# Optimization experiments

Measured on AMD Instinct MI355X. Metric: run time of the kernel, lower is better.

The kernel has to match this reference:

```python
import jax, jax.numpy as jnp
import numpy as np

NHEAD = 6
EPS = 1.1920929e-07  # torch RMSNorm default eps = finfo(float32).eps


def _rms(x, g):
    return x * jax.lax.rsqrt(jnp.mean(x * x, axis=-1, keepdims=True) + EPS) * g


def _mha(q, k, v):
    # q: [B, Sq, Hq, D]; k, v: [B, Sk, Hk, D] with Hk == Hq or Hk == 1 (broadcast)
    d = q.shape[-1]
    qh = q.transpose(0, 2, 1, 3)            # [B, Hq, Sq, D]
    kh = k.transpose(0, 2, 1, 3)            # [B, Hk, Sk, D]
    vh = v.transpose(0, 2, 1, 3)
    s = jnp.matmul(qh, kh.transpose(0, 1, 3, 2)) * (1.0 / np.sqrt(d).astype(np.float32))
    a = jax.nn.softmax(s, axis=-1)
    return jnp.matmul(a, vh).transpose(0, 2, 1, 3)  # [B, Sq, Hq, D]


def setup_inputs() -> dict:
    key = jax.random.key(0)
    B, R, G, E, L = 4, 1024, 8, 192, 4
    F = 2 * E  # dim_feedforward = emsize * 2
    ks = jax.random.split(key, 12)

    def w(k, shape):
        return jax.random.normal(k, shape, jnp.float32) * 0.02

    return {
        "hidden": jax.random.normal(ks[0], (B, R, G, E), jnp.float32),
        "Wq1": w(ks[1], (L, E, E)), "Wk1": w(ks[2], (L, E, E)),
        "Wv1": w(ks[3], (L, E, E)), "Wo1": w(ks[4], (L, E, E)),
        "Wq2": w(ks[5], (L, E, E)), "Wk2": w(ks[6], (L, E, E)),
        "Wv2": w(ks[7], (L, E, E)), "Wo2": w(ks[8], (L, E, E)),
        "W1": w(ks[9], (L, E, F)), "W2": w(ks[10], (L, F, E)),
        "g1": jnp.ones((L, E), jnp.float32),
        "g2": jnp.ones((L, E), jnp.float32),
        "g3": jnp.ones((L, E), jnp.float32),
        "single_eval_pos": 768,
    }


def reference(hidden, Wq1, Wk1, Wv1, Wo1, Wq2, Wk2, Wv2, Wo2, W1, W2, g1, g2, g3, single_eval_pos):
    B, R, G, E = hidden.shape
    H, D = NHEAD, E // NHEAD
    sep = int(single_eval_pos)
    L = Wq1.shape[0]
    x = hidden
    for i in range(L):
        # --- per-sample attention between feature groups: seqs of length G ---
        xf = x.reshape(B * R, G, E)
        q = (xf @ Wq1[i]).reshape(B * R, G, H, D)
        k = (xf @ Wk1[i]).reshape(B * R, G, H, D)
        v = (xf @ Wv1[i]).reshape(B * R, G, H, D)
        xf = xf + _mha(q, k, v).reshape(B * R, G, E) @ Wo1[i]
        # --- along-column attention over rows with train/test split ---
        xr = _rms(xf, g1[i]).reshape(B, R, G, E).transpose(0, 2, 1, 3).reshape(B * G, R, E)
        q = (xr @ Wq2[i]).reshape(B * G, R, H, D)
        k = (xr[:, :sep] @ Wk2[i]).reshape(B * G, sep, H, D)
        v = (xr[:, :sep] @ Wv2[i]).reshape(B * G, sep, H, D)
        train_out = _mha(q[:, :sep], k, v)
        # test rows attend to first head's keys/values only (broadcast over heads)
        test_out = _mha(q[:, sep:], k[:, :, :1], v[:, :, :1])
        attn = jnp.concatenate([train_out, test_out], axis=1).reshape(B * G, R, E) @ Wo2[i]
        xc = _rms(xr + attn, g2[i])
        # --- MLP (exact GELU) + final RMSNorm ---
        x = xc.reshape(B, G, R, E).transpose(0, 2, 1, 3)
        x = x + jax.nn.gelu(x @ W1[i], approximate=False) @ W2[i]
        x = _rms(x, g3[i])
    return x
```

## Files before the change

kernel.cpp:

```cpp
#include <hip/hip_runtime.h>
#include <hip/hip_bf16.h>
#include <math.h>

#define B_ 4
#define R_ 1024
#define G_ 8
#define E_ 192
#define H_ 6
#define D_ 32
#define L_ 4
#define F_ 384
#define M_ (B_*R_*G_)
static const size_t NBUF = (size_t)M_ * E_;
static const size_t WPL  = 8 * (size_t)E_ * E_ + 2 * (size_t)E_ * F_;

typedef __attribute__((ext_vector_type(8))) short bf16x8;
typedef __attribute__((ext_vector_type(8))) unsigned short u16x8;
typedef __attribute__((ext_vector_type(4))) float f32x4;

__device__ __forceinline__ float gelu_exact(float x) {
    return 0.5f * x * (1.0f + erff(x * 0.7071067811865475f));
}
__device__ __forceinline__ unsigned short f2bf(float f) {
    __hip_bfloat16 h = __float2bfloat16(f);
    return *(unsigned short*)&h;
}
__device__ __forceinline__ float bf2f(unsigned short h) {
    union { unsigned u; float f; } v; v.u = ((unsigned)h) << 16; return v.f;
}
__device__ __forceinline__ bf16x8 mk8(unsigned long long lo, unsigned long long hi) {
    union { unsigned long long q[2]; bf16x8 v; } u;
    u.q[0] = lo; u.q[1] = hi; return u.v;
}

__global__ __launch_bounds__(256)
void k_convw_all(const float* __restrict__ Wq1, const float* __restrict__ Wk1,
                 const float* __restrict__ Wv1, const float* __restrict__ Wo1,
                 const float* __restrict__ Wq2, const float* __restrict__ Wk2,
                 const float* __restrict__ Wv2, const float* __restrict__ Wo2,
                 const float* __restrict__ W1,  const float* __restrict__ W2,
                 unsigned short* __restrict__ Wt)
{
    const int t = blockIdx.x;
    const int layer = t / 432;
    const int r = t % 432;
    const float* src; unsigned short* dst; int K, N; float scale = 1.f; int tile;
    if (r < 288) {
        const int w = r / 36; tile = r % 36; K = E_; N = E_;
        const float* tab[8] = {Wq1, Wk1, Wv1, Wo1, Wq2, Wk2, Wv2, Wo2};
        src = tab[w] + (size_t)layer * E_ * E_;
        dst = Wt + (size_t)layer * WPL + (size_t)w * E_ * E_;
        if (w == 0) scale = 0.17677669529663687f;
        if (w == 4) scale = 0.17677669529663687f * 1.4426950408889634f;
    } else if (r < 360) {
        tile = r - 288; K = E_; N = F_;
        src = W1 + (size_t)layer * E_ * F_;
        dst = Wt + (size_t)layer * WPL + 8 * (size_t)E_ * E_;
    } else {
        tile = r - 360; K = F_; N = E_;
        src = W2 + (size_t)layer * E_ * F_;
        dst = Wt + (size_t)layer * WPL + 8 * (size_t)E_ * E_ + (size_t)E_ * F_;
    }
    const int ntx = N / 32;
    const int kb = (tile / ntx) * 32, nb = (tile % ntx) * 32;
    __shared__ float tl[32][33];
    const int tx = threadIdx.x & 31, ty = threadIdx.x >> 5;
    for (int i2 = 0; i2 < 32; i2 += 8)
        tl[ty + i2][tx] = src[(size_t)(kb + ty + i2) * N + nb + tx];
    __syncthreads();
    for (int i2 = 0; i2 < 32; i2 += 8)
        dst[(size_t)(nb + ty + i2) * K + kb + tx] = f2bf(tl[tx][ty + i2] * scale);
}

template<bool ABF16, int EPI>
__global__ __launch_bounds__(256)
void k_gemm_mfma(const void* __restrict__ Ap, const unsigned short* __restrict__ Wt,
                 void* __restrict__ Cp, int ldc, int K)
{
    __shared__ unsigned short As[64][40];
    __shared__ unsigned short Bs[192][40];
    const int m0 = blockIdx.x * 64;
    const int n0 = blockIdx.y * 192;
    const int tid = threadIdx.x;
    const int w = tid >> 6, lane = tid & 63, l15 = lane & 15, g = lane >> 4;
    const int arow = tid >> 2, akoff = (tid & 3) << 3;
    f32x4 acc[4][3];
#pragma unroll
    for (int mt = 0; mt < 4; ++mt)
#pragma unroll
        for (int nt = 0; nt < 3; ++nt)
#pragma unroll
            for (int r2 = 0; r2 < 4; ++r2) acc[mt][nt][r2] = 0.f;
    const int nK = K >> 5;

    float4 ax, ay; u16x8 av; u16x8 bv0, bv1, bv2;
    auto gload = [&](int k0) {
        if (ABF16) {
            av = *(const u16x8*)((const unsigned short*)Ap + (size_t)(m0 + arow) * K + k0 + akoff);
        } else {
            const float* ap = (const float*)Ap + (size_t)(m0 + arow) * K + k0 + akoff;
            ax = *(const float4*)ap; ay = *(const float4*)(ap + 4);
        }
        bv0 = *(const u16x8*)(Wt + (size_t)(n0 + arow      ) * K + k0 + akoff);
        bv1 = *(const u16x8*)(Wt + (size_t)(n0 + arow +  64) * K + k0 + akoff);
        bv2 = *(const u16x8*)(Wt + (size_t)(n0 + arow + 128) * K + k0 + akoff);
    };
    auto swrite = [&]() {
        u16x8 aw;
        if (ABF16) aw = av;
        else {
            aw[0] = f2bf(ax.x); aw[1] = f2bf(ax.y); aw[2] = f2bf(ax.z); aw[3] = f2bf(ax.w);
            aw[4] = f2bf(ay.x); aw[5] = f2bf(ay.y); aw[6] = f2bf(ay.z); aw[7] = f2bf(ay.w);
        }
        *(u16x8*)&As[arow][akoff] = aw;
        *(u16x8*)&Bs[arow][akoff] = bv0;
        *(u16x8*)&Bs[arow + 64][akoff] = bv1;
        *(u16x8*)&Bs[arow + 128][akoff] = bv2;
    };

    gload(0);
    for (int kc = 0; kc < nK; ++kc) {
        __syncthreads();
        swrite();
        __syncthreads();
        if (kc + 1 < nK) gload((kc + 1) << 5);
        bf16x8 af[4], bfr[3];
#pragma unroll
        for (int mt = 0; mt < 4; ++mt) af[mt] = *(const bf16x8*)&As[mt * 16 + l15][g * 8];
#pragma unroll
        for (int nt = 0; nt < 3; ++nt) bfr[nt] = *(const bf16x8*)&Bs[w * 48 + nt * 16 + l15][g * 8];
#pragma unroll
        for (int mt = 0; mt < 4; ++mt)
#pragma unroll
            for (int nt = 0; nt < 3; ++nt)
                acc[mt][nt] = __builtin_amdgcn_mfma_f32_16x16x32_bf16(af[mt], bfr[nt], acc[mt][nt], 0, 0, 0);
    }

#pragma unroll
    for (int mt = 0; mt < 4; ++mt)
#pragma unroll
        for (int r2 = 0; r2 < 4; ++r2) {
            const int m = m0 + mt * 16 + g * 4 + r2;
#pragma unroll
            for (int nt = 0; nt < 3; ++nt) {
                const int n = w * 48 + nt * 16 + l15;
                float v = acc[mt][nt][r2];
                if (EPI == 1) v = gelu_exact(v);
                ((unsigned short*)Cp)[(size_t)m * ldc + n0 + n] = f2bf(v);
            }
        }
}

template<bool RESBF16, int EPI>
__global__ __launch_bounds__(256)
void k_gemm_rms32(const unsigned short* __restrict__ Ap, const unsigned short* __restrict__ Wt,
                  const void* __restrict__ Resp, const float* __restrict__ gvec,
                  void* __restrict__ Cp, int K)
{
    __shared__ unsigned short As[32][40];
    __shared__ unsigned short Bs[192][40];
    __shared__ float ss_red[4][16];
    const int m0 = blockIdx.x * 32;
    const int tid = threadIdx.x;
    const int w = tid >> 6, lane = tid & 63, l15 = lane & 15, g = lane >> 4;
    const int mt = w & 1, nh = w >> 1;
    const int arow = tid >> 2, akoff = (tid & 3) << 3;
    f32x4 acc[6];
#pragma unroll
    for (int nt = 0; nt < 6; ++nt)
#pragma unroll
        for (int r2 = 0; r2 < 4; ++r2) acc[nt][r2] = 0.f;
    const int nK = K >> 5;

    u16x8 av, bv0, bv1, bv2;
    auto gload = [&](int k0) {
        if (tid < 128)
            av = *(const u16x8*)(Ap + (size_t)(m0 + arow) * K + k0 + akoff);
        bv0 = *(const u16x8*)(Wt + (size_t)(arow      ) * K + k0 + akoff);
        bv1 = *(const u16x8*)(Wt + (size_t)(arow +  64) * K + k0 + akoff);
        bv2 = *(const u16x8*)(Wt + (size_t)(arow + 128) * K + k0 + akoff);
    };
    auto swrite = [&]() {
        if (tid < 128) *(u16x8*)&As[arow][akoff] = av;
        *(u16x8*)&Bs[arow][akoff] = bv0;
        *(u16x8*)&Bs[arow + 64][akoff] = bv1;
        *(u16x8*)&Bs[arow + 128][akoff] = bv2;
    };

    gload(0);
    for (int kc = 0; kc < nK; ++kc) {
        __syncthreads();
        swrite();
        __syncthreads();
        if (kc + 1 < nK) gload((kc + 1) << 5);
        bf16x8 af = *(const bf16x8*)&As[mt * 16 + l15][g * 8];
        bf16x8 bfr[6];
#pragma unroll
        for (int nt = 0; nt < 6; ++nt) bfr[nt] = *(const bf16x8*)&Bs[nh * 96 + nt * 16 + l15][g * 8];
#pragma unroll
        for (int nt = 0; nt < 6; ++nt)
            acc[nt] = __builtin_amdgcn_mfma_f32_16x16x32_bf16(af, bfr[nt], acc[nt], 0, 0, 0);
    }

    float ssp[4] = {0.f, 0.f, 0.f, 0.f};
#pragma unroll
    for (int r2 = 0; r2 < 4; ++r2) {
        const int m = m0 + mt * 16 + g * 4 + r2;
#pragma unroll
        for (int nt = 0; nt < 6; ++nt) {
            const int n = nh * 96 + nt * 16 + l15;
            float rres = RESBF16 ? bf2f(((const unsigned short*)Resp)[(size_t)m * E_ + n])
                                 : ((const float*)Resp)[(size_t)m * E_ + n];
            float v = acc[nt][r2] + rres;
            acc[nt][r2] = v;
            ssp[r2] += v * v;
        }
    }
#pragma unroll
    for (int off = 1; off < 16; off <<= 1)
#pragma unroll
        for (int r2 = 0; r2 < 4; ++r2)
            ssp[r2] += __shfl_xor(ssp[r2], off);
    if (l15 == 0) {
#pragma unroll
        for (int r2 = 0; r2 < 4; ++r2)
            ss_red[w][g * 4 + r2] = ssp[r2];
    }
    __syncthreads();
#pragma unroll
    for (int r2 = 0; r2 < 4; ++r2) {
        const int lr = g * 4 + r2;
        const float ss = ss_red[mt][lr] + ss_red[2 + mt][lr];
        const float inv = rsqrtf(ss * (1.0f / 192.0f) + 1.1920929e-07f);
        const int m = m0 + mt * 16 + lr;
        size_t orow;
        if (EPI == 2) {
            const int b = m >> 13, rr = (m >> 3) & 1023, gg = m & 7;
            orow = (((size_t)b * G_ + gg) << 10) + rr;
        } else if (EPI == 3) {
            const int b = m >> 13, gg = (m >> 10) & 7, rr = m & 1023;
            orow = ((((size_t)b << 10) + rr) << 3) + gg;
        } else {
            orow = m;
        }
#pragma unroll
        for (int nt = 0; nt < 6; ++nt) {
            const int n = nh * 96 + nt * 16 + l15;
            const float v = acc[nt][r2] * inv * gvec[n];
            if (EPI == 4) ((float*)Cp)[orow * E_ + n] = v;
            else          ((unsigned short*)Cp)[orow * E_ + n] = f2bf(v);
        }
    }
}

template<bool AF32>
__global__ __launch_bounds__(256)
void k_featblock(const void* __restrict__ Xin, const unsigned short* __restrict__ Wqkv,
                 const unsigned short* __restrict__ Wo, const float* __restrict__ gvec,
                 unsigned short* __restrict__ Ynb)
{
    __shared__ __align__(16) unsigned char raw[576 * 40 * 2];
    __shared__ __align__(16) unsigned short As[32][40];
    __shared__ __align__(16) unsigned short Tl[32][200];
    __shared__ float ss_red[4][32];

    unsigned short (*Bq)[40]    = (unsigned short (*)[40])raw;
    unsigned short (*QKVl)[584] = (unsigned short (*)[584])raw;
    unsigned short (*Bo)[40]    = (unsigned short (*)[40])raw;

    const int m0 = blockIdx.x * 32;
    const int tid = threadIdx.x;
    const int w = tid >> 6, lane = tid & 63, l15 = lane & 15, g = lane >> 4;
    const int arow = (tid & 127) >> 2, akoff = (tid & 3) << 3;

    f32x4 acc[2][9];
#pragma unroll
    for (int mt = 0; mt < 2; ++mt)
#pragma unroll
        for (int nt = 0; nt < 9; ++nt)
#pragma unroll
            for (int r2 = 0; r2 < 4; ++r2) acc[mt][nt][r2] = 0.f;

    u16x8 av; u16x8 bv[9];
    auto gload1 = [&](int k0) {
        if (tid < 128) {
            if (AF32) {
                const float* ap = (const float*)Xin + (size_t)(m0 + arow) * E_ + k0 + akoff;
                float4 x = *(const float4*)ap, y = *(const float4*)(ap + 4);
                av[0] = f2bf(x.x); av[1] = f2bf(x.y); av[2] = f2bf(x.z); av[3] = f2bf(x.w);
                av[4] = f2bf(y.x); av[5] = f2bf(y.y); av[6] = f2bf(y.z); av[7] = f2bf(y.w);
            } else {
                av = *(const u16x8*)((const unsigned short*)Xin + (size_t)(m0 + arow) * E_ + k0 + akoff);
            }
        }
#pragma unroll
        for (int j = 0; j < 9; ++j) {
            const int v = tid + 256 * j;
            bv[j] = *(const u16x8*)(Wqkv + (size_t)(v >> 2) * E_ + k0 + ((v & 3) << 3));
        }
    };
    auto swrite1 = [&]() {
        if (tid < 128) *(u16x8*)&As[arow][akoff] = av;
#pragma unroll
        for (int j = 0; j < 9; ++j) {
            const int v = tid + 256 * j;
            *(u16x8*)&Bq[v >> 2][(v & 3) << 3] = bv[j];
        }
    };

    gload1(0);
    for (int kc = 0; kc < 6; ++kc) {
        __syncthreads();
        swrite1();
        __syncthreads();
        if (kc + 1 < 6) gload1((kc + 1) << 5);
        bf16x8 af0 = *(const bf16x8*)&As[l15][g * 8];
        bf16x8 af1 = *(const bf16x8*)&As[16 + l15][g * 8];
#pragma unroll
        for (int nt = 0; nt < 9; ++nt) {
            bf16x8 bf = *(const bf16x8*)&Bq[w * 144 + nt * 16 + l15][g * 8];
            acc[0][nt] = __builtin_amdgcn_mfma_f32_16x16x32_bf16(af0, bf, acc[0][nt], 0, 0, 0);
            acc[1][nt] = __builtin_amdgcn_mfma_f32_16x16x32_bf16(af1, bf, acc[1][nt], 0, 0, 0);
        }
    }
    __syncthreads();
#pragma unroll
    for (int mt = 0; mt < 2; ++mt)
#pragma unroll
        for (int r2 = 0; r2 < 4; ++r2)
#pragma unroll
            for (int nt = 0; nt < 9; ++nt)
                QKVl[mt * 16 + g * 4 + r2][w * 144 + nt * 16 + l15] = f2bf(acc[mt][nt][r2]);

    u16x8 bo[3];
    auto gload3 = [&](int k0) {
#pragma unroll
        for (int j = 0; j < 3; ++j) {
            const int v = tid + 256 * j;
            bo[j] = *(const u16x8*)(Wo + (size_t)(v >> 2) * E_ + k0 + ((v & 3) << 3));
        }
    };
    gload3(0);
    __syncthreads();

    {
        const int i = lane >> 3, j = lane & 7;
        const int r0 = w * 8;
#pragma unroll
        for (int h = 0; h < 6; ++h) {
            float s = 0.f;
#pragma unroll
            for (int d8 = 0; d8 < 4; ++d8) {
                u16x8 qv = *(const u16x8*)&QKVl[r0 + i][h * 32 + d8 * 8];
                u16x8 kv = *(const u16x8*)&QKVl[r0 + j][192 + h * 32 + d8 * 8];
#pragma unroll
                for (int e = 0; e < 8; ++e) s += bf2f(qv[e]) * bf2f(kv[e]);
            }
            float mx = s;
#pragma unroll
            for (int off = 1; off < 8; off <<= 1) mx = fmaxf(mx, __shfl_xor(mx, off));
            float p = __expf(s - mx);
            float sum = p;
#pragma unroll
            for (int off = 1; off < 8; off <<= 1) sum += __shfl_xor(sum, off);
            p /= sum;
            const int base = lane & ~7;
            float o0 = 0.f, o1 = 0.f, o2 = 0.f, o3 = 0.f;
#pragma unroll
            for (int jj = 0; jj < 8; ++jj) {
                float pj = __shfl(p, base + jj);
                ushort4 vv = *(const ushort4*)&QKVl[r0 + jj][384 + h * 32 + j * 4];
                o0 += pj * bf2f(vv.x); o1 += pj * bf2f(vv.y);
                o2 += pj * bf2f(vv.z); o3 += pj * bf2f(vv.w);
            }
            ushort4 ov; ov.x = f2bf(o0); ov.y = f2bf(o1); ov.z = f2bf(o2); ov.w = f2bf(o3);
            *(ushort4*)&Tl[r0 + i][h * 32 + j * 4] = ov;
        }
    }

    float rv[2][4][3];
#pragma unroll
    for (int mt = 0; mt < 2; ++mt)
#pragma unroll
        for (int r2 = 0; r2 < 4; ++r2) {
            const int m = m0 + mt * 16 + g * 4 + r2;
#pragma unroll
            for (int nt = 0; nt < 3; ++nt) {
                const int n = w * 48 + nt * 16 + l15;
                rv[mt][r2][nt] = AF32 ? ((const float*)Xin)[(size_t)m * E_ + n]
                                      : bf2f(((const unsigned short*)Xin)[(size_t)m * E_ + n]);
            }
        }
    __syncthreads();

    f32x4 acc2[2][3];
#pragma unroll
    for (int mt = 0; mt < 2; ++mt)
#pragma unroll
        for (int nt = 0; nt < 3; ++nt)
#pragma unroll
            for (int r2 = 0; r2 < 4; ++r2) acc2[mt][nt][r2] = 0.f;

    for (int kc = 0; kc < 6; ++kc) {
        __syncthreads();
#pragma unroll
        for (int j = 0; j < 3; ++j) {
            const int v = tid + 256 * j;
            *(u16x8*)&Bo[v >> 2][(v & 3) << 3] = bo[j];
        }
        __syncthreads();
        if (kc + 1 < 6) gload3((kc + 1) << 5);
        const int k0 = kc << 5;
        bf16x8 af0 = *(const bf16x8*)&Tl[l15][k0 + g * 8];
        bf16x8 af1 = *(const bf16x8*)&Tl[16 + l15][k0 + g * 8];
#pragma unroll
        for (int nt = 0; nt < 3; ++nt) {
            bf16x8 bf = *(const bf16x8*)&Bo[w * 48 + nt * 16 + l15][g * 8];
            acc2[0][nt] = __builtin_amdgcn_mfma_f32_16x16x32_bf16(af0, bf, acc2[0][nt], 0, 0, 0);
            acc2[1][nt] = __builtin_amdgcn_mfma_f32_16x16x32_bf16(af1, bf, acc2[1][nt], 0, 0, 0);
        }
    }
    __syncthreads();

    float ssp[2][4] = {};
#pragma unroll
    for (int mt = 0; mt < 2; ++mt)
#pragma unroll
        for (int r2 = 0; r2 < 4; ++r2) {
#pragma unroll
            for (int nt = 0; nt < 3; ++nt) {
                float v = acc2[mt][nt][r2] + rv[mt][r2][nt];
                acc2[mt][nt][r2] = v;
                ssp[mt][r2] += v * v;
            }
        }
#pragma unroll
    for (int off = 1; off < 16; off <<= 1)
#pragma unroll
        for (int mt = 0; mt < 2; ++mt)
#pragma unroll
            for (int r2 = 0; r2 < 4; ++r2)
                ssp[mt][r2] += __shfl_xor(ssp[mt][r2], off);
    if (l15 == 0) {
#pragma unroll
        for (int mt = 0; mt < 2; ++mt)
#pragma unroll
            for (int r2 = 0; r2 < 4; ++r2)
                ss_red[w][mt * 16 + g * 4 + r2] = ssp[mt][r2];
    }
    __syncthreads();
#pragma unroll
    for (int mt = 0; mt < 2; ++mt)
#pragma unroll
        for (int r2 = 0; r2 < 4; ++r2) {
            const int row = mt * 16 + g * 4 + r2;
            const float ss = ss_red[0][row] + ss_red[1][row] + ss_red[2][row] + ss_red[3][row];
            const float inv = rsqrtf(ss * (1.0f / 192.0f) + 1.1920929e-07f);
            const int m = m0 + row;
            const int b = m >> 13, rr = (m >> 3) & 1023, gg = m & 7;
            const size_t orow = (((size_t)(b * G_ + gg)) << 10) + rr;
#pragma unroll
            for (int nt = 0; nt < 3; ++nt) {
                const int n = w * 48 + nt * 16 + l15;
                Ynb[orow * E_ + n] = f2bf(acc2[mt][nt][r2] * inv * gvec[n]);
            }
        }
}

__global__ __launch_bounds__(256)
void k_attn2(const unsigned short* __restrict__ QKV, unsigned short* __restrict__ T,
             const int* __restrict__ sep_ptr)
{
    __shared__ __align__(16) unsigned short K_lds[64][40];
    __shared__ __align__(16) unsigned short V_lds[2048];

    const int sep = *sep_ptr;
    const int bid = blockIdx.x;
    const int sh = ((bid >> 7) << 3) | (bid & 7);
    const int qtile = (bid >> 3) & 15;
    const int s = sh / H_, h = sh % H_;
    const int q0 = qtile * 64;

    const int tid = threadIdx.x;
    const int w = tid >> 6;
    const int lane = tid & 63;
    const int l15 = lane & 15;
    const int g = lane >> 4;

    const int qrow = q0 + w * 16 + l15;
    u16x8 qf = *(const u16x8*)(QKV + ((size_t)s * R_ + qrow) * 576 + h * D_ + g * 8);

    u16x8 onesu;
#pragma unroll
    for (int e = 0; e < 8; ++e) onesu[e] = 0x3F80;
    const bf16x8 onesf = (bf16x8)onesu;

    const bool lo = (q0 < sep);
    const bool hi = (q0 + 64 > sep);
    const int npass = (lo && hi) ? 2 : 1;
    const int nChunk = (sep + 63) >> 6;

    const int skey = tid >> 2;
    const int sg   = tid & 3;
    const int vst = ((sg >> 1) * 16 + (skey >> 2)) * 64 + (skey & 3) * 16 + (sg & 1) * 8;
    const unsigned vaddr = (unsigned)(size_t)&V_lds[0] + (unsigned)(g * 128 + l15 * 2);

    for (int pass = 0; pass < npass; ++pass) {
        const int hk = (pass == 0) ? (lo ? h : 0) : 0;
        const unsigned short* Kb = QKV + (size_t)s * R_ * 576 + 192 + hk * D_;
        const unsigned short* Vb = QKV + (size_t)s * R_ * 576 + 384 + hk * D_;

        f32x4 o0 = {0.f, 0.f, 0.f, 0.f};
        f32x4 o1 = {0.f, 0.f, 0.f, 0.f};
        f32x4 o2 = {0.f, 0.f, 0.f, 0.f};

        u16x8 kv_k = *(const u16x8*)(Kb + (size_t)skey * 576 + sg * 8);
        u16x8 kv_v = *(const u16x8*)(Vb + (size_t)skey * 576 + sg * 8);

        for (int kc = 0; kc < nChunk; ++kc) {
            const int kbase = kc * 64;
            const bool full = (kbase + 64 <= sep);
            __syncthreads();
            *(u16x8*)&K_lds[skey][sg * 8] = kv_k;
            *(u16x8*)&V_lds[vst] = kv_v;
            __syncthreads();
            if (kc + 1 < nChunk) {
                kv_k = *(const u16x8*)(Kb + (size_t)(kbase + 64 + skey) * 576 + sg * 8);
                kv_v = *(const u16x8*)(Vb + (size_t)(kbase + 64 + skey) * 576 + sg * 8);
            }

            f32x4 sc[4];
            const f32x4 zf = {0.f, 0.f, 0.f, 0.f};
            __builtin_amdgcn_s_setprio(1);
#pragma unroll
            for (int t = 0; t < 4; ++t) {
                bf16x8 a = *(const bf16x8*)&K_lds[t * 16 + l15][g * 8];
                sc[t] = __builtin_amdgcn_mfma_f32_16x16x32_bf16(a, (bf16x8)qf, zf, 0, 0, 0);
            }
            __builtin_amdgcn_s_setprio(0);
            if (!full) {
#pragma unroll
                for (int t = 0; t < 4; ++t)
#pragma unroll
                    for (int r = 0; r < 4; ++r)
                        if (kbase + t * 16 + g * 4 + r >= sep) sc[t][r] = -1e30f;
            }
            bf16x8 pb0, pb1;
            {
                u16x8 p0, p1;
#pragma unroll
                for (int r = 0; r < 4; ++r) {
                    p0[r]     = f2bf(exp2f(sc[0][r]));
                    p0[4 + r] = f2bf(exp2f(sc[1][r]));
                    p1[r]     = f2bf(exp2f(sc[2][r]));
                    p1[4 + r] = f2bf(exp2f(sc[3][r]));
                }
                pb0 = (bf16x8)p0; pb1 = (bf16x8)p1;
            }
            unsigned long long t0, t1, t2, t3, t4, t5, t6, t7;
            asm volatile(
                "ds_read_b64_tr_b16 %0, %8 offset:0\n\t"
                "ds_read_b64_tr_b16 %1, %8 offset:512\n\t"
                "ds_read_b64_tr_b16 %2, %8 offset:1024\n\t"
                "ds_read_b64_tr_b16 %3, %8 offset:1536\n\t"
                "ds_read_b64_tr_b16 %4, %8 offset:2048\n\t"
                "ds_read_b64_tr_b16 %5, %8 offset:2560\n\t"
                "ds_read_b64_tr_b16 %6, %8 offset:3072\n\t"
                "ds_read_b64_tr_b16 %7, %8 offset:3584\n\t"
                "s_waitcnt lgkmcnt(0)"
                : "=&v"(t0), "=&v"(t1), "=&v"(t2), "=&v"(t3),
                  "=&v"(t4), "=&v"(t5), "=&v"(t6), "=&v"(t7)
                : "v"(vaddr)
                : "memory");
            __builtin_amdgcn_sched_barrier(0);
            __builtin_amdgcn_s_setprio(1);
            o0 = __builtin_amdgcn_mfma_f32_16x16x32_bf16(mk8(t0, t1), pb0, o0, 0, 0, 0);
            o1 = __builtin_amdgcn_mfma_f32_16x16x32_bf16(mk8(t4, t5), pb0, o1, 0, 0, 0);
            o2 = __builtin_amdgcn_mfma_f32_16x16x32_bf16(onesf,       pb0, o2, 0, 0, 0);
            o0 = __builtin_amdgcn_mfma_f32_16x16x32_bf16(mk8(t2, t3), pb1, o0, 0, 0, 0);
            o1 = __builtin_amdgcn_mfma_f32_16x16x32_bf16(mk8(t6, t7), pb1, o1, 0, 0, 0);
            o2 = __builtin_amdgcn_mfma_f32_16x16x32_bf16(onesf,       pb1, o2, 0, 0, 0);
            __builtin_amdgcn_s_setprio(0);
        }

        const bool valid = (npass == 1) || (pass == 0 ? (qrow < sep) : (qrow >= sep));
        if (valid) {
            const float inv = 1.f / o2[0];
            unsigned short* tp = T + ((size_t)s * R_ + qrow) * E_ + h * D_;
            ushort4 v0, v1;
            v0.x = f2bf(o0[0] * inv); v0.y = f2bf(o0[1] * inv);
            v0.z = f2bf(o0[2] * inv); v0.w = f2bf(o0[3] * inv);
            v1.x = f2bf(o1[0] * inv); v1.y = f2bf(o1[1] * inv);
            v1.z = f2bf(o1[2] * inv); v1.w = f2bf(o1[3] * inv);
            *(ushort4*)(tp + g * 4)      = v0;
            *(ushort4*)(tp + 16 + g * 4) = v1;
        }
    }
}

extern "C" void kernel_launch(void* const* d_in, const int* in_sizes, int n_in,
                              void* d_out, int out_size, void* d_ws, size_t ws_size,
                              hipStream_t stream) {
    const float* hidden = (const float*)d_in[0];
    const float* Wq1 = (const float*)d_in[1];
    const float* Wk1 = (const float*)d_in[2];
    const float* Wv1 = (const float*)d_in[3];
    const float* Wo1 = (const float*)d_in[4];
    const float* Wq2 = (const float*)d_in[5];
    const float* Wk2 = (const float*)d_in[6];
    const float* Wv2 = (const float*)d_in[7];
    const float* Wo2 = (const float*)d_in[8];
    const float* W1  = (const float*)d_in[9];
    const float* W2  = (const float*)d_in[10];
    const float* g1  = (const float*)d_in[11];
    const float* g2  = (const float*)d_in[12];
    const float* g3  = (const float*)d_in[13];
    const int*   sep = (const int*)d_in[14];

    float* Xout = (float*)d_out;
    unsigned short* ws = (unsigned short*)d_ws;
    unsigned short* QKVb = ws;
    unsigned short* Tb   = QKVb + (size_t)M_ * 576;
    unsigned short* Ynb  = Tb + NBUF;
    unsigned short* Xcb  = Ynb + NBUF;
    unsigned short* Xb   = Xcb + NBUF;
    unsigned short* Wt   = Xb + NBUF;
    unsigned short* H1b  = QKVb;

    const dim3 blk(256);
    const dim3 gQKV(M_ / 64, 3);
    const dim3 gW1(M_ / 64, 2);
    const dim3 g32(M_ / 32);
    const dim3 gA2(32 * H_ * 16);

    k_convw_all<<<dim3(432 * L_), blk, 0, stream>>>(Wq1, Wk1, Wv1, Wo1, Wq2, Wk2, Wv2, Wo2, W1, W2, Wt);

    for (int i = 0; i < L_; ++i) {
        unsigned short* wl = Wt + (size_t)i * WPL;
        const unsigned short* wqkv1 = wl;
        const unsigned short* wo1   = wl + 3 * (size_t)E_ * E_;
        const unsigned short* wqkv2 = wl + 4 * (size_t)E_ * E_;
        const unsigned short* wo2   = wl + 7 * (size_t)E_ * E_;
        const unsigned short* w1    = wl + 8 * (size_t)E_ * E_;
        const unsigned short* w2    = wl + 8 * (size_t)E_ * E_ + (size_t)E_ * F_;
        const float* g1i = g1 + (size_t)i * E_;
        const float* g2i = g2 + (size_t)i * E_;
        const float* g3i = g3 + (size_t)i * E_;

        if (i == 0)
            k_featblock<true><<<g32, blk, 0, stream>>>(hidden, wqkv1, wo1, g1i, Ynb);
        else
            k_featblock<false><<<g32, blk, 0, stream>>>(Xb, wqkv1, wo1, g1i, Ynb);
        k_gemm_mfma<true, 0><<<gQKV, blk, 0, stream>>>(Ynb, wqkv2, QKVb, 576, E_);
        k_attn2<<<gA2, blk, 0, stream>>>(QKVb, Tb, sep);
        k_gemm_rms32<true, 3><<<g32, blk, 0, stream>>>(Tb, wo2, Ynb, g2i, Xcb, E_);
        k_gemm_mfma<true, 1><<<gW1, blk, 0, stream>>>(Xcb, w1, H1b, F_, E_);
        if (i == L_ - 1)
            k_gemm_rms32<true, 4><<<g32, blk, 0, stream>>>(H1b, w2, Xcb, g3i, Xout, F_);
        else
            k_gemm_rms32<true, 5><<<g32, blk, 0, stream>>>(H1b, w2, Xcb, g3i, Xb, F_);
    }
}
```

Measured before the change: 624.1 us.

## Give each wave a private LDS weight slice and drop block barriers in featblock GEMMs

The feature-attention kernel now stages the whole 32x192 activation tile into LDS once. Each wave then loads and stores only its own slice of the QKV and output-projection weights into a private LDS region. Because no wave reads another wave's slice, the two __syncthreads per K-step in both GEMM loops go away, and weight prefetch runs two stages ahead with B fragments held in registers. The activation tile buffer is reused for the attention output, and the RMS reduction scratch is carved out of the shared raw buffer. This relies on in-order LDS access within a wave for the write-after-read on each slice.

```diff
diff --git a/kernel.cpp b/kernel.cpp
--- a/kernel.cpp
+++ b/kernel.cpp
@@ -259,19 +259,30 @@
                  const unsigned short* __restrict__ Wo, const float* __restrict__ gvec,
                  unsigned short* __restrict__ Ynb)
 {
-    __shared__ __align__(16) unsigned char raw[576 * 40 * 2];
-    __shared__ __align__(16) unsigned short As[32][40];
-    __shared__ __align__(16) unsigned short Tl[32][200];
-    __shared__ float ss_red[4][32];
-
-    unsigned short (*Bq)[40]    = (unsigned short (*)[40])raw;
+    __shared__ __align__(16) unsigned short raw[23040];
+    __shared__ __align__(16) unsigned short AsTl[32][200];
+
     unsigned short (*QKVl)[584] = (unsigned short (*)[584])raw;
-    unsigned short (*Bo)[40]    = (unsigned short (*)[40])raw;
-
     const int m0 = blockIdx.x * 32;
     const int tid = threadIdx.x;
     const int w = tid >> 6, lane = tid & 63, l15 = lane & 15, g = lane >> 4;
-    const int arow = (tid & 127) >> 2, akoff = (tid & 3) << 3;
+
+#pragma unroll
+    for (int j = 0; j < 3; ++j) {
+        const int v = tid + 256 * j;
+        const int row = v / 24, ch = v % 24;
+        u16x8 aw;
+        if (AF32) {
+            const float* ap = (const float*)Xin + (size_t)(m0 + row) * E_ + ch * 8;
+            float4 x = *(const float4*)ap, y = *(const float4*)(ap + 4);
+            aw[0] = f2bf(x.x); aw[1] = f2bf(x.y); aw[2] = f2bf(x.z); aw[3] = f2bf(x.w);
+            aw[4] = f2bf(y.x); aw[5] = f2bf(y.y); aw[6] = f2bf(y.z); aw[7] = f2bf(y.w);
+        } else {
+            aw = *(const u16x8*)((const unsigned short*)Xin + (size_t)(m0 + row) * E_ + ch * 8);
+        }
+        *(u16x8*)&AsTl[row][ch * 8] = aw;
+    }
+    __syncthreads();
 
     f32x4 acc[2][9];
 #pragma unroll
@@ -281,49 +292,45 @@
 #pragma unroll
             for (int r2 = 0; r2 < 4; ++r2) acc[mt][nt][r2] = 0.f;
 
-    u16x8 av; u16x8 bv[9];
+    unsigned short* slice1 = raw + w * 5760;
+    u16x8 bv[9];
     auto gload1 = [&](int k0) {
-        if (tid < 128) {
-            if (AF32) {
-                const float* ap = (const float*)Xin + (size_t)(m0 + arow) * E_ + k0 + akoff;
-                float4 x = *(const float4*)ap, y = *(const float4*)(ap + 4);
-                av[0] = f2bf(x.x); av[1] = f2bf(x.y); av[2] = f2bf(x.z); av[3] = f2bf(x.w);
-                av[4] = f2bf(y.x); av[5] = f2bf(y.y); av[6] = f2bf(y.z); av[7] = f2bf(y.w);
-            } else {
-                av = *(const u16x8*)((const unsigned short*)Xin + (size_t)(m0 + arow) * E_ + k0 + akoff);
-            }
-        }
 #pragma unroll
         for (int j = 0; j < 9; ++j) {
-            const int v = tid + 256 * j;
-            bv[j] = *(const u16x8*)(Wqkv + (size_t)(v >> 2) * E_ + k0 + ((v & 3) << 3));
+            const int v = lane + 64 * j;
+            bv[j] = *(const u16x8*)(Wqkv + (size_t)(w * 144 + (v >> 2)) * E_ + k0 + ((v & 3) << 3));
         }
     };
     auto swrite1 = [&]() {
-        if (tid < 128) *(u16x8*)&As[arow][akoff] = av;
 #pragma unroll
         for (int j = 0; j < 9; ++j) {
-            const int v = tid + 256 * j;
-            *(u16x8*)&Bq[v >> 2][(v & 3) << 3] = bv[j];
+            const int v = lane + 64 * j;
+            *(u16x8*)&slice1[(v >> 2) * 40 + ((v & 3) << 3)] = bv[j];
         }
     };
 
     gload1(0);
+    swrite1();
+    gload1(32);
+#pragma unroll
     for (int kc = 0; kc < 6; ++kc) {
-        __syncthreads();
-        swrite1();
-        __syncthreads();
-        if (kc + 1 < 6) gload1((kc + 1) << 5);
-        bf16x8 af0 = *(const bf16x8*)&As[l15][g * 8];
-        bf16x8 af1 = *(const bf16x8*)&As[16 + l15][g * 8];
+        const int k0 = kc << 5;
+        bf16x8 af0 = *(const bf16x8*)&AsTl[l15][k0 + g * 8];
+        bf16x8 af1 = *(const bf16x8*)&AsTl[16 + l15][k0 + g * 8];
+        bf16x8 bfr[9];
+#pragma unroll
+        for (int nt = 0; nt < 9; ++nt)
+            bfr[nt] = *(const bf16x8*)&slice1[(nt * 16 + l15) * 40 + g * 8];
 #pragma unroll
         for (int nt = 0; nt < 9; ++nt) {
-            bf16x8 bf = *(const bf16x8*)&Bq[w * 144 + nt * 16 + l15][g * 8];
-            acc[0][nt] = __builtin_amdgcn_mfma_f32_16x16x32_bf16(af0, bf, acc[0][nt], 0, 0, 0);
-            acc[1][nt] = __builtin_amdgcn_mfma_f32_16x16x32_bf16(af1, bf, acc[1][nt], 0, 0, 0);
-        }
+            acc[0][nt] = __builtin_amdgcn_mfma_f32_16x16x32_bf16(af0, bfr[nt], acc[0][nt], 0, 0, 0);
+            acc[1][nt] = __builtin_amdgcn_mfma_f32_16x16x32_bf16(af1, bfr[nt], acc[1][nt], 0, 0, 0);
+        }
+        if (kc + 1 < 6) swrite1();
+        if (kc + 2 < 6) gload1((kc + 2) << 5);
     }
     __syncthreads();
+
 #pragma unroll
     for (int mt = 0; mt < 2; ++mt)
 #pragma unroll
@@ -336,8 +343,8 @@
     auto gload3 = [&](int k0) {
 #pragma unroll
         for (int j = 0; j < 3; ++j) {
-            const int v = tid + 256 * j;
-            bo[j] = *(const u16x8*)(Wo + (size_t)(v >> 2) * E_ + k0 + ((v & 3) << 3));
+            const int v = lane + 64 * j;
+            bo[j] = *(const u16x8*)(Wo + (size_t)(w * 48 + (v >> 2)) * E_ + k0 + ((v & 3) << 3));
         }
     };
     gload3(0);
@@ -374,7 +381,7 @@
                 o2 += pj * bf2f(vv.z); o3 += pj * bf2f(vv.w);
             }
             ushort4 ov; ov.x = f2bf(o0); ov.y = f2bf(o1); ov.z = f2bf(o2); ov.w = f2bf(o3);
-            *(ushort4*)&Tl[r0 + i][h * 32 + j * 4] = ov;
+            *(ushort4*)&AsTl[r0 + i][h * 32 + j * 4] = ov;
         }
     }
 
@@ -393,6 +400,7 @@
         }
     __syncthreads();
 
+    unsigned short* slice3 = raw + w * 1920;
     f32x4 acc2[2][3];
 #pragma unroll
     for (int mt = 0; mt < 2; ++mt)
@@ -401,27 +409,34 @@
 #pragma unroll
             for (int r2 = 0; r2 < 4; ++r2) acc2[mt][nt][r2] = 0.f;
 
+    auto swrite3 = [&]() {
+#pragma unroll
+        for (int j = 0; j < 3; ++j) {
+            const int v = lane + 64 * j;
+            *(u16x8*)&slice3[(v >> 2) * 40 + ((v & 3) << 3)] = bo[j];
+        }
+    };
+    swrite3();
+    gload3(32);
+#pragma unroll
     for (int kc = 0; kc < 6; ++kc) {
-        __syncthreads();
-#pragma unroll
-        for (int j = 0; j < 3; ++j) {
-            const int v = tid + 256 * j;
-            *(u16x8*)&Bo[v >> 2][(v & 3) << 3] = bo[j];
-        }
-        __syncthreads();
-        if (kc + 1 < 6) gload3((kc + 1) << 5);
         const int k0 = kc << 5;
-        bf16x8 af0 = *(const bf16x8*)&Tl[l15][k0 + g * 8];
-        bf16x8 af1 = *(const bf16x8*)&Tl[16 + l15][k0 + g * 8];
+        bf16x8 af0 = *(const bf16x8*)&AsTl[l15][k0 + g * 8];
+        bf16x8 af1 = *(const bf16x8*)&AsTl[16 + l15][k0 + g * 8];
+        bf16x8 bfr[3];
+#pragma unroll
+        for (int nt = 0; nt < 3; ++nt)
+            bfr[nt] = *(const bf16x8*)&slice3[(nt * 16 + l15) * 40 + g * 8];
 #pragma unroll
         for (int nt = 0; nt < 3; ++nt) {
-            bf16x8 bf = *(const bf16x8*)&Bo[w * 48 + nt * 16 + l15][g * 8];
-            acc2[0][nt] = __builtin_amdgcn_mfma_f32_16x16x32_bf16(af0, bf, acc2[0][nt], 0, 0, 0);
-            acc2[1][nt] = __builtin_amdgcn_mfma_f32_16x16x32_bf16(af1, bf, acc2[1][nt], 0, 0, 0);
-        }
-    }
-    __syncthreads();
-
+            acc2[0][nt] = __builtin_amdgcn_mfma_f32_16x16x32_bf16(af0, bfr[nt], acc2[0][nt], 0, 0, 0);
+            acc2[1][nt] = __builtin_amdgcn_mfma_f32_16x16x32_bf16(af1, bfr[nt], acc2[1][nt], 0, 0, 0);
+        }
+        if (kc + 1 < 6) swrite3();
+        if (kc + 2 < 6) gload3((kc + 2) << 5);
+    }
+
+    float* S = (float*)(raw + 7680);
     float ssp[2][4] = {};
 #pragma unroll
     for (int mt = 0; mt < 2; ++mt)
@@ -446,7 +461,7 @@
         for (int mt = 0; mt < 2; ++mt)
 #pragma unroll
             for (int r2 = 0; r2 < 4; ++r2)
-                ss_red[w][mt * 16 + g * 4 + r2] = ssp[mt][r2];
+                S[w * 32 + mt * 16 + g * 4 + r2] = ssp[mt][r2];
     }
     __syncthreads();
 #pragma unroll
@@ -454,7 +469,7 @@
 #pragma unroll
         for (int r2 = 0; r2 < 4; ++r2) {
             const int row = mt * 16 + g * 4 + r2;
-            const float ss = ss_red[0][row] + ss_red[1][row] + ss_red[2][row] + ss_red[3][row];
+            const float ss = S[row] + S[32 + row] + S[64 + row] + S[96 + row];
             const float inv = rsqrtf(ss * (1.0f / 192.0f) + 1.1920929e-07f);
             const int m = m0 + row;
             const int b = m >> 13, rr = (m >> 3) & 1023, gg = m & 7;
```

After: 614.4 us. No clear change (-1.6%).
